# Optimization experiments

Measured on AMD Instinct MI355X. Metric: run time of the kernel, lower is better.

## Reference

```python
import jax, jax.numpy as jnp
import numpy as np

T, B, N, N2 = 2048, 32, 1024, 512

def setup_inputs() -> dict:
    key = jax.random.key(0)
    ks = jax.random.split(key, 7)
    s_n = 1.0 / np.sqrt(N)
    s_n2 = 1.0 / np.sqrt(N2)
    return {
        "hyp": jax.random.normal(ks[0], (T, B, N), dtype=jnp.float32),
        "W_w": jax.random.uniform(ks[1], (N2, N), jnp.float32, -s_n, s_n),
        "W_b": jax.random.uniform(ks[2], (N2,), jnp.float32, -s_n, s_n),
        "Wm_w": jax.random.uniform(ks[3], (N2, N), jnp.float32, -s_n, s_n),
        "Wm_b": jax.random.uniform(ks[4], (N2,), jnp.float32, -s_n, s_n),
        "Wh_w": jax.random.uniform(ks[5], (1, N2), jnp.float32, -s_n2, s_n2),
        "Wh_b": jax.random.uniform(ks[6], (1,), jnp.float32, -s_n2, s_n2),
        "dan_hidden_size": N,
        "attention_hidden_size": N2,
    }

def reference(hyp, W_w, W_b, Wm_w, Wm_b, Wh_w, Wh_b, dan_hidden_size, attention_hidden_size):
    # attention_type == 'attention' branch
    m = jnp.mean(hyp, axis=0)                      # [B, N] mean over time
    x = jnp.transpose(hyp, (1, 0, 2))              # [B, T, N]
    hq = jnp.tanh(jnp.einsum('btn,kn->btk', x, W_w) + W_b)        # [B, T, N2]
    hm = jnp.tanh(m @ Wm_w.T + Wm_b)[:, None, :]   # [B, 1, N2]
    h = hq * hm                                    # [B, T, N2]
    score = jnp.einsum('btk,ok->bto', h, Wh_w) + Wh_b  # [B, T, 1]
    a = jax.nn.softmax(score, axis=1)              # softmax over T
    c = jnp.sum(a * x, axis=1)                     # [B, N]
    return c
```

## Files before the change

### kernel.cpp

```cpp
#include <hip/hip_runtime.h>
#include <hip/hip_bf16.h>

#define TDIM 2048
#define BDIM 32
#define NDIM 1024
#define N2DIM 512
#define BN (BDIM * NDIM)
#define LDSP 72

typedef float f32x4 __attribute__((ext_vector_type(4)));
typedef __bf16 bf16x8 __attribute__((ext_vector_type(8)));

__device__ __forceinline__ float bf2f(unsigned int u) {
    union { unsigned int i; float f; } c;
    c.i = (u & 0xffffu) << 16;
    return c.f;
}

__device__ __forceinline__ unsigned short f2bf(float f) {
    union { float f; unsigned int i; } c;
    c.f = f;
    unsigned int i = c.i;
    unsigned int r = (i >> 16) & 1u;
    i += 0x7fffu + r;
    return (unsigned short)(i >> 16);
}

__device__ __forceinline__ int detect_f32(const void* wb) {
    const unsigned short* p = (const unsigned short*)wb;
    int cnt = 0;
    #pragma unroll
    for (int i = 0; i < 64; ++i) cnt += ((p[i] & 0x7fffu) <= 0x3D00u) ? 1 : 0;
    return cnt != 64;
}

__device__ __forceinline__ float ldf(const void* p, size_t i, int isf32) {
    if (isf32) return ((const float*)p)[i];
    return bf2f(((const unsigned short*)p)[i]);
}

__device__ __forceinline__ float tanh_fast(float x) {
    float e = __expf(2.0f * x);
    return 1.0f - 2.0f / (e + 1.0f);
}

__device__ __forceinline__ void unpack8(uint4 u, float* f) {
    f[0] = bf2f(u.x); f[1] = bf2f(u.x >> 16);
    f[2] = bf2f(u.y); f[3] = bf2f(u.y >> 16);
    f[4] = bf2f(u.z); f[5] = bf2f(u.z >> 16);
    f[6] = bf2f(u.w); f[7] = bf2f(u.w >> 16);
}

__device__ __forceinline__ void async16(const void* g, void* l) {
    __builtin_amdgcn_global_load_lds(
        (const __attribute__((address_space(1))) void*)g,
        (__attribute__((address_space(3))) void*)l, 16, 0, 0);
}


__global__ __launch_bounds__(256) void k_mean_cvt(const void* __restrict__ hyp,
                                                  const void* __restrict__ wb,
                                                  unsigned short* __restrict__ hyp16,
                                                  float* __restrict__ part) {
    const int isf32 = detect_f32(wb);
    const int col4 = (blockIdx.x * 256 + threadIdx.x) * 4;
    const int tc   = blockIdx.y;
    float a0 = 0.f, a1 = 0.f, a2 = 0.f, a3 = 0.f;
    if (isf32) {
        const float* h = (const float*)hyp + (size_t)(tc * 128) * BN + col4;
        unsigned short* o = hyp16 + (size_t)(tc * 128) * BN + col4;
        #pragma unroll 4
        for (int tt = 0; tt < 128; ++tt) {
            float4 v = *(const float4*)(h + (size_t)tt * BN);
            a0 += v.x; a1 += v.y; a2 += v.z; a3 += v.w;
            ushort4 u = { f2bf(v.x), f2bf(v.y), f2bf(v.z), f2bf(v.w) };
            *(ushort4*)(o + (size_t)tt * BN) = u;
        }
    } else {
        const unsigned short* h = (const unsigned short*)hyp + (size_t)(tc * 128) * BN + col4;
        unsigned short* o = hyp16 + (size_t)(tc * 128) * BN + col4;
        #pragma unroll 4
        for (int tt = 0; tt < 128; ++tt) {
            ushort4 u = *(const ushort4*)(h + (size_t)tt * BN);
            *(ushort4*)(o + (size_t)tt * BN) = u;
            a0 += bf2f(u.x); a1 += bf2f(u.y); a2 += bf2f(u.z); a3 += bf2f(u.w);
        }
    }
    float4 r = { a0, a1, a2, a3 };
    *(float4*)(part + (size_t)tc * BN + col4) = r;
}

__global__ __launch_bounds__(256) void k_reduce_mean(const float* __restrict__ part,
                                                     float* __restrict__ m) {
    int i4 = (blockIdx.x * 256 + threadIdx.x) * 4;
    float4 s = { 0.f, 0.f, 0.f, 0.f };
    #pragma unroll
    for (int c = 0; c < 16; ++c) {
        float4 v = *(const float4*)(part + (size_t)c * BN + i4);
        s.x += v.x; s.y += v.y; s.z += v.z; s.w += v.w;
    }
    float k = 1.0f / (float)TDIM;
    float4 r = { s.x * k, s.y * k, s.z * k, s.w * k };
    *(float4*)(m + i4) = r;
}

__global__ __launch_bounds__(256) void k_cvtW(const void* __restrict__ W_w,
                                              const void* __restrict__ wb,
                                              unsigned short* __restrict__ W16) {
    const int isf32 = detect_f32(wb);
    int i4 = (blockIdx.x * 256 + threadIdx.x) * 4;
    if (isf32) {
        float4 v = *(const float4*)((const float*)W_w + i4);
        ushort4 u = { f2bf(v.x), f2bf(v.y), f2bf(v.z), f2bf(v.w) };
        *(ushort4*)(W16 + i4) = u;
    } else {
        *(ushort4*)(W16 + i4) = *(const ushort4*)((const unsigned short*)W_w + i4);
    }
}

__global__ __launch_bounds__(256) void k_g(const float* __restrict__ m,
                                           const void* __restrict__ Wm_w,
                                           const void* __restrict__ Wm_b,
                                           const void* __restrict__ Wh_w,
                                           const void* __restrict__ wb,
                                           float* __restrict__ g) {
    const int isf32 = detect_f32(wb);
    int wid  = (blockIdx.x * 256 + threadIdx.x) >> 6;
    int lane = threadIdx.x & 63;
    int b = wid >> 9;
    int k = wid & 511;
    const float* mr = m + (size_t)b * NDIM;
    float s = 0.f;
    for (int i = lane; i < NDIM; i += 64)
        s += mr[i] * ldf(Wm_w, (size_t)k * NDIM + i, isf32);
    #pragma unroll
    for (int off = 32; off > 0; off >>= 1) s += __shfl_down(s, off, 64);
    if (lane == 0) {
        float v = tanh_fast(s + ldf(Wm_b, k, isf32));
        g[(size_t)b * N2DIM + k] = v * ldf(Wh_w, k, isf32);
    }
}

__global__ __launch_bounds__(256) void k_score(const unsigned short* __restrict__ hyp16,
                                               const unsigned short* __restrict__ W16,
                                               const void* __restrict__ W_b,
                                               const float* __restrict__ g,
                                               float* __restrict__ score) {
    __shared__ __align__(16) unsigned short sA[128 * 64];
    __shared__ __align__(16) unsigned short sW[128 * 64];
    __shared__ float sRed[2][128];

    const int isf32 = detect_f32(W_b);
    const int tid = threadIdx.x;
    const int l   = tid & 63;
    const int w   = tid >> 6;
    const int wt  = w & 1;
    const int wkk = w >> 1;
    const int lm  = l & 15;
    const int lq  = l >> 4;
    const int b   = blockIdx.y;
    const int t0  = blockIdx.x * 128;

    const int grow = l >> 3;
    const int gkq  = (l & 7) ^ grow;
    const int swz0 = ((lq)     ^ (lm & 7)) * 8;
    const int swz1 = ((4 + lq) ^ (lm & 7)) * 8;

    float scoreAcc[4][4];
    #pragma unroll
    for (int mi = 0; mi < 4; ++mi)
        #pragma unroll
        for (int r = 0; r < 4; ++r) scoreAcc[mi][r] = 0.f;

    for (int kblk = 0; kblk < 4; ++kblk) {
        f32x4 acc[4][4];
        #pragma unroll
        for (int mi = 0; mi < 4; ++mi)
            #pragma unroll
            for (int ni = 0; ni < 4; ++ni) {
                f32x4 z = {0.f, 0.f, 0.f, 0.f};
                acc[mi][ni] = z;
            }

        for (int it = 0; it < 16; ++it) {
            const int n0 = it * 64;
            #pragma unroll
            for (int p = 0; p < 4; ++p) {
                const int row = (w * 4 + p) * 8 + grow;
                async16(hyp16 + (size_t)(t0 + row) * BN + b * NDIM + n0 + gkq * 8,
                        &sA[(w * 4 + p) * 512]);
                async16(W16 + (size_t)(kblk * 128 + row) * NDIM + n0 + gkq * 8,
                        &sW[(w * 4 + p) * 512]);
            }
            __syncthreads();

            #pragma unroll
            for (int kk = 0; kk < 2; ++kk) {
                const int swz = kk ? swz1 : swz0;
                bf16x8 af[4];
                #pragma unroll
                for (int mi = 0; mi < 4; ++mi) {
                    int mrow = wt * 64 + mi * 16 + lm;
                    af[mi] = *(const bf16x8*)&sA[mrow * 64 + swz];
                }
                #pragma unroll
                for (int ni = 0; ni < 4; ++ni) {
                    int nrow = wkk * 64 + ni * 16 + lm;
                    bf16x8 bfr = *(const bf16x8*)&sW[nrow * 64 + swz];
                    #pragma unroll
                    for (int mi = 0; mi < 4; ++mi)
                        acc[mi][ni] = __builtin_amdgcn_mfma_f32_16x16x32_bf16(
                            af[mi], bfr, acc[mi][ni], 0, 0, 0);
                }
            }
            __syncthreads();
        }

        #pragma unroll
        for (int ni = 0; ni < 4; ++ni) {
            int kc = kblk * 128 + wkk * 64 + ni * 16 + lm;
            float wbv = ldf(W_b, kc, isf32);
            float gg  = g[(size_t)b * N2DIM + kc];
            #pragma unroll
            for (int mi = 0; mi < 4; ++mi)
                #pragma unroll
                for (int r = 0; r < 4; ++r) {
                    float v = tanh_fast(acc[mi][ni][r] + wbv);
                    scoreAcc[mi][r] += v * gg;
                }
        }
    }

    #pragma unroll
    for (int mi = 0; mi < 4; ++mi)
        #pragma unroll
        for (int r = 0; r < 4; ++r) {
            float s = scoreAcc[mi][r];
            s += __shfl_xor(s, 1, 64);
            s += __shfl_xor(s, 2, 64);
            s += __shfl_xor(s, 4, 64);
            s += __shfl_xor(s, 8, 64);
            if (lm == 0) sRed[wkk][wt * 64 + mi * 16 + lq * 4 + r] = s;
        }
    __syncthreads();
    if (tid < 128) {
        score[(size_t)b * TDIM + t0 + tid] = sRed[0][tid] + sRed[1][tid];
    }
}

__global__ __launch_bounds__(256) void k_softmax(const float* __restrict__ score,
                                                 float* __restrict__ a) {
    __shared__ float red[8];
    int b = blockIdx.x;
    int tid = threadIdx.x;
    int w = tid >> 6, l = tid & 63;
    const float* s = score + (size_t)b * TDIM;
    float v[8];
    float mx = -1e30f;
    #pragma unroll
    for (int i = 0; i < 8; ++i) { v[i] = s[tid + i * 256]; mx = fmaxf(mx, v[i]); }
    #pragma unroll
    for (int off = 32; off > 0; off >>= 1) mx = fmaxf(mx, __shfl_xor(mx, off, 64));
    if (l == 0) red[w] = mx;
    __syncthreads();
    mx = fmaxf(fmaxf(red[0], red[1]), fmaxf(red[2], red[3]));
    float sum = 0.f;
    #pragma unroll
    for (int i = 0; i < 8; ++i) { v[i] = __expf(v[i] - mx); sum += v[i]; }
    #pragma unroll
    for (int off = 32; off > 0; off >>= 1) sum += __shfl_xor(sum, off, 64);
    if (l == 0) red[4 + w] = sum;
    __syncthreads();
    sum = red[4] + red[5] + red[6] + red[7];
    float inv = 1.0f / sum;
    float* ap = a + (size_t)b * TDIM;
    #pragma unroll
    for (int i = 0; i < 8; ++i) ap[tid + i * 256] = v[i] * inv;
}

__global__ __launch_bounds__(256) void k_wsum_part(const unsigned short* __restrict__ hyp16,
                                                   const float* __restrict__ a,
                                                   float* __restrict__ part) {
    const int col8 = (blockIdx.x * 256 + threadIdx.x) * 8;
    const int tc   = blockIdx.y;
    const int b    = col8 >> 10;
    const float* av = a + (size_t)b * TDIM + tc * 128;
    const uint4* src = (const uint4*)(hyp16 + (size_t)(tc * 128) * BN + col8);
    float acc[8] = {0.f,0.f,0.f,0.f,0.f,0.f,0.f,0.f};
    #pragma unroll 4
    for (int tt = 0; tt < 128; ++tt) {
        float wgt = av[tt];
        uint4 u = src[(size_t)tt * (BN / 8)];
        float f[8]; unpack8(u, f);
        #pragma unroll
        for (int j = 0; j < 8; ++j) acc[j] += wgt * f[j];
    }
    float* dst = part + (size_t)tc * BN + col8;
    #pragma unroll
    for (int j = 0; j < 8; ++j) dst[j] = acc[j];
}

__global__ __launch_bounds__(256) void k_reduce_out(const float* __restrict__ part,
                                                    const void* __restrict__ wb,
                                                    void* __restrict__ out) {
    const int isf32 = detect_f32(wb);
    int i4 = (blockIdx.x * 256 + threadIdx.x) * 4;
    float4 s = { 0.f, 0.f, 0.f, 0.f };
    #pragma unroll
    for (int c = 0; c < 16; ++c) {
        float4 v = *(const float4*)(part + (size_t)c * BN + i4);
        s.x += v.x; s.y += v.y; s.z += v.z; s.w += v.w;
    }
    if (isf32) {
        *(float4*)((float*)out + i4) = s;
    } else {
        ushort4 u = { f2bf(s.x), f2bf(s.y), f2bf(s.z), f2bf(s.w) };
        *(ushort4*)((unsigned short*)out + i4) = u;
    }
}

__global__ __launch_bounds__(256) void k_mean_fb(const void* __restrict__ hyp,
                                                 const void* __restrict__ wb,
                                                 float* __restrict__ m) {
    const int isf32 = detect_f32(wb);
    int i = blockIdx.x * 256 + threadIdx.x;
    float s = 0.f;
    if (isf32) {
        const float* h = (const float*)hyp;
        #pragma unroll 8
        for (int t = 0; t < TDIM; ++t) s += h[(size_t)t * BN + i];
    } else {
        const unsigned short* h = (const unsigned short*)hyp;
        #pragma unroll 8
        for (int t = 0; t < TDIM; ++t) s += bf2f(h[(size_t)t * BN + i]);
    }
    m[i] = s * (1.0f / (float)TDIM);
}

__global__ __launch_bounds__(256) void k_score_fb(const void* __restrict__ hyp,
                                                  const void* __restrict__ W_w,
                                                  const void* __restrict__ W_b,
                                                  const float* __restrict__ g,
                                                  float* __restrict__ score) {
    __shared__ __align__(16) unsigned short sA[128 * LDSP];
    __shared__ __align__(16) unsigned short sW[128 * LDSP];
    __shared__ float sRed[2][128];

    const int isf32 = detect_f32(W_b);
    const int tid = threadIdx.x;
    const int l   = tid & 63;
    const int w   = tid >> 6;
    const int wt  = w & 1;
    const int wkk = w >> 1;
    const int lm  = l & 15;
    const int lq  = l >> 4;
    const int b   = blockIdx.y;
    const int t0  = blockIdx.x * 128;

    float scoreAcc[4][4];
    #pragma unroll
    for (int mi = 0; mi < 4; ++mi)
        #pragma unroll
        for (int r = 0; r < 4; ++r) scoreAcc[mi][r] = 0.f;

    for (int kblk = 0; kblk < 4; ++kblk) {
        f32x4 acc[4][4];
        #pragma unroll
        for (int mi = 0; mi < 4; ++mi)
            #pragma unroll
            for (int ni = 0; ni < 4; ++ni) {
                f32x4 z = {0.f, 0.f, 0.f, 0.f};
                acc[mi][ni] = z;
            }
        for (int it = 0; it < 16; ++it) {
            const int n0 = it * 64;
            #pragma unroll
            for (int p = 0; p < 4; ++p) {
                int ch  = p * 256 + tid;
                int row = ch >> 3;
                int pos = ch & 7;
                size_t offA = (size_t)(t0 + row) * BN + b * NDIM + n0 + pos * 8;
                size_t offW = (size_t)(kblk * 128 + row) * NDIM + n0 + pos * 8;
                uint4 va, vw;
                if (isf32) {
                    const float4* fa = (const float4*)((const float*)hyp + offA);
                    float4 a0 = fa[0], a1 = fa[1];
                    va.x = f2bf(a0.x) | ((unsigned)f2bf(a0.y) << 16);
                    va.y = f2bf(a0.z) | ((unsigned)f2bf(a0.w) << 16);
                    va.z = f2bf(a1.x) | ((unsigned)f2bf(a1.y) << 16);
                    va.w = f2bf(a1.z) | ((unsigned)f2bf(a1.w) << 16);
                    const float4* fw = (const float4*)((const float*)W_w + offW);
                    float4 w0 = fw[0], w1 = fw[1];
                    vw.x = f2bf(w0.x) | ((unsigned)f2bf(w0.y) << 16);
                    vw.y = f2bf(w0.z) | ((unsigned)f2bf(w0.w) << 16);
                    vw.z = f2bf(w1.x) | ((unsigned)f2bf(w1.y) << 16);
                    vw.w = f2bf(w1.z) | ((unsigned)f2bf(w1.w) << 16);
                } else {
                    va = *(const uint4*)((const unsigned short*)hyp + offA);
                    vw = *(const uint4*)((const unsigned short*)W_w + offW);
                }
                *(uint4*)&sA[row * LDSP + pos * 8] = va;
                *(uint4*)&sW[row * LDSP + pos * 8] = vw;
            }
            __syncthreads();
            #pragma unroll
            for (int kk = 0; kk < 2; ++kk) {
                const int koff = kk * 32 + lq * 8;
                bf16x8 af[4];
                #pragma unroll
                for (int mi = 0; mi < 4; ++mi) {
                    int mrow = wt * 64 + mi * 16 + lm;
                    af[mi] = *(const bf16x8*)&sA[mrow * LDSP + koff];
                }
                #pragma unroll
                for (int ni = 0; ni < 4; ++ni) {
                    int nrow = wkk * 64 + ni * 16 + lm;
                    bf16x8 bfr = *(const bf16x8*)&sW[nrow * LDSP + koff];
                    #pragma unroll
                    for (int mi = 0; mi < 4; ++mi)
                        acc[mi][ni] = __builtin_amdgcn_mfma_f32_16x16x32_bf16(
                            af[mi], bfr, acc[mi][ni], 0, 0, 0);
                }
            }
            __syncthreads();
        }
        #pragma unroll
        for (int ni = 0; ni < 4; ++ni) {
            int kc = kblk * 128 + wkk * 64 + ni * 16 + lm;
            float wbv = ldf(W_b, kc, isf32);
            float gg  = g[(size_t)b * N2DIM + kc];
            #pragma unroll
            for (int mi = 0; mi < 4; ++mi)
                #pragma unroll
                for (int r = 0; r < 4; ++r) {
                    float v = tanh_fast(acc[mi][ni][r] + wbv);
                    scoreAcc[mi][r] += v * gg;
                }
        }
    }
    #pragma unroll
    for (int mi = 0; mi < 4; ++mi)
        #pragma unroll
        for (int r = 0; r < 4; ++r) {
            float s = scoreAcc[mi][r];
            s += __shfl_xor(s, 1, 64);
            s += __shfl_xor(s, 2, 64);
            s += __shfl_xor(s, 4, 64);
            s += __shfl_xor(s, 8, 64);
            if (lm == 0) sRed[wkk][wt * 64 + mi * 16 + lq * 4 + r] = s;
        }
    __syncthreads();
    if (tid < 128) {
        score[(size_t)b * TDIM + t0 + tid] = sRed[0][tid] + sRed[1][tid];
    }
}

__global__ __launch_bounds__(256) void k_wsum_fb(const void* __restrict__ hyp,
                                                 const float* __restrict__ a,
                                                 const void* __restrict__ wb,
                                                 void* __restrict__ out) {
    const int isf32 = detect_f32(wb);
    int i = blockIdx.x * 256 + threadIdx.x;
    int b = i >> 10;
    const float* av = a + (size_t)b * TDIM;
    float s = 0.f;
    if (isf32) {
        const float* h = (const float*)hyp;
        #pragma unroll 8
        for (int t = 0; t < TDIM; ++t) s += av[t] * h[(size_t)t * BN + i];
    } else {
        const unsigned short* h = (const unsigned short*)hyp;
        #pragma unroll 8
        for (int t = 0; t < TDIM; ++t) s += av[t] * bf2f(h[(size_t)t * BN + i]);
    }
    if (isf32) ((float*)out)[i] = s;
    else       ((unsigned short*)out)[i] = f2bf(s);
}

extern "C" void kernel_launch(void* const* d_in, const int* in_sizes, int n_in,
                              void* d_out, int out_size, void* d_ws, size_t ws_size,
                              hipStream_t stream) {
    const void* hyp  = d_in[0];
    const void* W_w  = d_in[1];
    const void* W_b  = d_in[2];
    const void* Wm_w = d_in[3];
    const void* Wm_b = d_in[4];
    const void* Wh_w = d_in[5];

    float* ws    = (float*)d_ws;
    float* m     = ws;
    float* g     = m + BN;
    float* score = g + BDIM * N2DIM;
    float* a     = score + BDIM * TDIM;
    float* part  = a + BDIM * TDIM;
    unsigned short* W16   = (unsigned short*)(part + 16 * BN);
    unsigned short* hyp16 = W16 + (size_t)N2DIM * NDIM;
    const size_t need = 138084352ull;

    if (ws_size >= need) {
        k_mean_cvt  <<<dim3(32, 16), 256, 0, stream>>>(hyp, W_b, hyp16, part);
        k_reduce_mean<<<dim3(32),    256, 0, stream>>>(part, m);
        k_cvtW      <<<dim3(512),    256, 0, stream>>>(W_w, W_b, W16);
        k_g         <<<dim3(4096),   256, 0, stream>>>(m, Wm_w, Wm_b, Wh_w, W_b, g);
        k_score     <<<dim3(16, 32), 256, 0, stream>>>(hyp16, W16, W_b, g, score);
        k_softmax   <<<dim3(32),     256, 0, stream>>>(score, a);
        k_wsum_part <<<dim3(16, 16), 256, 0, stream>>>(hyp16, a, part);
        k_reduce_out<<<dim3(32),     256, 0, stream>>>(part, W_b, d_out);
    } else {
        k_mean_fb   <<<dim3(128),    256, 0, stream>>>(hyp, W_b, m);
        k_g         <<<dim3(4096),   256, 0, stream>>>(m, Wm_w, Wm_b, Wh_w, W_b, g);
        k_score_fb  <<<dim3(16, 32), 256, 0, stream>>>(hyp, W_w, W_b, g, score);
        k_softmax   <<<dim3(32),     256, 0, stream>>>(score, a);
        k_wsum_fb   <<<dim3(128),    256, 0, stream>>>(hyp, a, W_b, d_out);
    }
}
```

Measured before the change: 564.1 us.

## Split score GEMM over hidden blocks and raise time-chunk partitions for occupancy

The score kernel grid gains a z dimension over the four hidden-size blocks. Each block writes a partial score, and the softmax kernel sums the four partials. The mean and weighted-sum kernels now use 64 time chunks instead of 16, so more blocks run concurrently, and the mean reduction is merged into the W conversion kernel, removing one launch. k_g also switches to vectorized float4 loads. The cost is more partial-sum traffic and a larger workspace, and hyp16 A-tiles are now reloaded by each z block.

```diff
diff --git a/kernel.cpp b/kernel.cpp
--- a/kernel.cpp
+++ b/kernel.cpp
@@ -7,6 +7,7 @@
 #define N2DIM 512
 #define BN (BDIM * NDIM)
 #define LDSP 72
+#define NPART 64
 
 typedef float f32x4 __attribute__((ext_vector_type(4)));
 typedef __bf16 bf16x8 __attribute__((ext_vector_type(8)));
@@ -67,20 +68,20 @@
     const int tc   = blockIdx.y;
     float a0 = 0.f, a1 = 0.f, a2 = 0.f, a3 = 0.f;
     if (isf32) {
-        const float* h = (const float*)hyp + (size_t)(tc * 128) * BN + col4;
-        unsigned short* o = hyp16 + (size_t)(tc * 128) * BN + col4;
-        #pragma unroll 4
-        for (int tt = 0; tt < 128; ++tt) {
+        const float* h = (const float*)hyp + (size_t)(tc * 32) * BN + col4;
+        unsigned short* o = hyp16 + (size_t)(tc * 32) * BN + col4;
+        #pragma unroll 8
+        for (int tt = 0; tt < 32; ++tt) {
             float4 v = *(const float4*)(h + (size_t)tt * BN);
             a0 += v.x; a1 += v.y; a2 += v.z; a3 += v.w;
             ushort4 u = { f2bf(v.x), f2bf(v.y), f2bf(v.z), f2bf(v.w) };
             *(ushort4*)(o + (size_t)tt * BN) = u;
         }
     } else {
-        const unsigned short* h = (const unsigned short*)hyp + (size_t)(tc * 128) * BN + col4;
-        unsigned short* o = hyp16 + (size_t)(tc * 128) * BN + col4;
-        #pragma unroll 4
-        for (int tt = 0; tt < 128; ++tt) {
+        const unsigned short* h = (const unsigned short*)hyp + (size_t)(tc * 32) * BN + col4;
+        unsigned short* o = hyp16 + (size_t)(tc * 32) * BN + col4;
+        #pragma unroll 8
+        for (int tt = 0; tt < 32; ++tt) {
             ushort4 u = *(const ushort4*)(h + (size_t)tt * BN);
             *(ushort4*)(o + (size_t)tt * BN) = u;
             a0 += bf2f(u.x); a1 += bf2f(u.y); a2 += bf2f(u.z); a3 += bf2f(u.w);
@@ -90,31 +91,32 @@
     *(float4*)(part + (size_t)tc * BN + col4) = r;
 }
 
-__global__ __launch_bounds__(256) void k_reduce_mean(const float* __restrict__ part,
-                                                     float* __restrict__ m) {
-    int i4 = (blockIdx.x * 256 + threadIdx.x) * 4;
-    float4 s = { 0.f, 0.f, 0.f, 0.f };
-    #pragma unroll
-    for (int c = 0; c < 16; ++c) {
-        float4 v = *(const float4*)(part + (size_t)c * BN + i4);
-        s.x += v.x; s.y += v.y; s.z += v.z; s.w += v.w;
-    }
-    float k = 1.0f / (float)TDIM;
-    float4 r = { s.x * k, s.y * k, s.z * k, s.w * k };
-    *(float4*)(m + i4) = r;
-}
-
-__global__ __launch_bounds__(256) void k_cvtW(const void* __restrict__ W_w,
+__global__ __launch_bounds__(256) void k_prep(const void* __restrict__ W_w,
                                               const void* __restrict__ wb,
-                                              unsigned short* __restrict__ W16) {
+                                              const float* __restrict__ part,
+                                              unsigned short* __restrict__ W16,
+                                              float* __restrict__ m) {
     const int isf32 = detect_f32(wb);
-    int i4 = (blockIdx.x * 256 + threadIdx.x) * 4;
-    if (isf32) {
-        float4 v = *(const float4*)((const float*)W_w + i4);
-        ushort4 u = { f2bf(v.x), f2bf(v.y), f2bf(v.z), f2bf(v.w) };
-        *(ushort4*)(W16 + i4) = u;
-    } else {
-        *(ushort4*)(W16 + i4) = *(const ushort4*)((const unsigned short*)W_w + i4);
+    if (blockIdx.x < 512) {
+        int i4 = (blockIdx.x * 256 + threadIdx.x) * 4;
+        if (isf32) {
+            float4 v = *(const float4*)((const float*)W_w + i4);
+            ushort4 u = { f2bf(v.x), f2bf(v.y), f2bf(v.z), f2bf(v.w) };
+            *(ushort4*)(W16 + i4) = u;
+        } else {
+            *(ushort4*)(W16 + i4) = *(const ushort4*)((const unsigned short*)W_w + i4);
+        }
+    } else {
+        int i4 = ((blockIdx.x - 512) * 256 + threadIdx.x) * 4;
+        float4 s = { 0.f, 0.f, 0.f, 0.f };
+        #pragma unroll
+        for (int c = 0; c < NPART; ++c) {
+            float4 v = *(const float4*)(part + (size_t)c * BN + i4);
+            s.x += v.x; s.y += v.y; s.z += v.z; s.w += v.w;
+        }
+        float k = 1.0f / (float)TDIM;
+        float4 r = { s.x * k, s.y * k, s.z * k, s.w * k };
+        *(float4*)(m + i4) = r;
     }
 }
 
@@ -131,8 +133,26 @@
     int k = wid & 511;
     const float* mr = m + (size_t)b * NDIM;
     float s = 0.f;
-    for (int i = lane; i < NDIM; i += 64)
-        s += mr[i] * ldf(Wm_w, (size_t)k * NDIM + i, isf32);
+    if (isf32) {
+        const float* wr = (const float*)Wm_w + (size_t)k * NDIM;
+        #pragma unroll
+        for (int i = 0; i < 4; ++i) {
+            int idx = (lane + i * 64) * 4;
+            float4 mv = *(const float4*)(mr + idx);
+            float4 wv = *(const float4*)(wr + idx);
+            s += mv.x * wv.x + mv.y * wv.y + mv.z * wv.z + mv.w * wv.w;
+        }
+    } else {
+        const unsigned short* wr = (const unsigned short*)Wm_w + (size_t)k * NDIM;
+        #pragma unroll
+        for (int i = 0; i < 4; ++i) {
+            int idx = (lane + i * 64) * 4;
+            float4 mv = *(const float4*)(mr + idx);
+            ushort4 wv = *(const ushort4*)(wr + idx);
+            s += mv.x * bf2f(wv.x) + mv.y * bf2f(wv.y)
+               + mv.z * bf2f(wv.z) + mv.w * bf2f(wv.w);
+        }
+    }
     #pragma unroll
     for (int off = 32; off > 0; off >>= 1) s += __shfl_down(s, off, 64);
     if (lane == 0) {
@@ -145,7 +165,7 @@
                                                const unsigned short* __restrict__ W16,
                                                const void* __restrict__ W_b,
                                                const float* __restrict__ g,
-                                               float* __restrict__ score) {
+                                               float* __restrict__ sp) {
     __shared__ __align__(16) unsigned short sA[128 * 64];
     __shared__ __align__(16) unsigned short sW[128 * 64];
     __shared__ float sRed[2][128];
@@ -160,75 +180,73 @@
     const int lq  = l >> 4;
     const int b   = blockIdx.y;
     const int t0  = blockIdx.x * 128;
+    const int kblk = blockIdx.z;
 
     const int grow = l >> 3;
     const int gkq  = (l & 7) ^ grow;
     const int swz0 = ((lq)     ^ (lm & 7)) * 8;
     const int swz1 = ((4 + lq) ^ (lm & 7)) * 8;
 
+    f32x4 acc[4][4];
+    #pragma unroll
+    for (int mi = 0; mi < 4; ++mi)
+        #pragma unroll
+        for (int ni = 0; ni < 4; ++ni) {
+            f32x4 z = {0.f, 0.f, 0.f, 0.f};
+            acc[mi][ni] = z;
+        }
+
+    for (int it = 0; it < 16; ++it) {
+        const int n0 = it * 64;
+        #pragma unroll
+        for (int p = 0; p < 4; ++p) {
+            const int row = (w * 4 + p) * 8 + grow;
+            async16(hyp16 + (size_t)(t0 + row) * BN + b * NDIM + n0 + gkq * 8,
+                    &sA[(w * 4 + p) * 512]);
+            async16(W16 + (size_t)(kblk * 128 + row) * NDIM + n0 + gkq * 8,
+                    &sW[(w * 4 + p) * 512]);
+        }
+        __syncthreads();
+
+        #pragma unroll
+        for (int kk = 0; kk < 2; ++kk) {
+            const int swz = kk ? swz1 : swz0;
+            bf16x8 af[4];
+            #pragma unroll
+            for (int mi = 0; mi < 4; ++mi) {
+                int mrow = wt * 64 + mi * 16 + lm;
+                af[mi] = *(const bf16x8*)&sA[mrow * 64 + swz];
+            }
+            #pragma unroll
+            for (int ni = 0; ni < 4; ++ni) {
+                int nrow = wkk * 64 + ni * 16 + lm;
+                bf16x8 bfr = *(const bf16x8*)&sW[nrow * 64 + swz];
+                #pragma unroll
+                for (int mi = 0; mi < 4; ++mi)
+                    acc[mi][ni] = __builtin_amdgcn_mfma_f32_16x16x32_bf16(
+                        af[mi], bfr, acc[mi][ni], 0, 0, 0);
+            }
+        }
+        __syncthreads();
+    }
+
     float scoreAcc[4][4];
     #pragma unroll
     for (int mi = 0; mi < 4; ++mi)
         #pragma unroll
         for (int r = 0; r < 4; ++r) scoreAcc[mi][r] = 0.f;
-
-    for (int kblk = 0; kblk < 4; ++kblk) {
-        f32x4 acc[4][4];
+    #pragma unroll
+    for (int ni = 0; ni < 4; ++ni) {
+        int kc = kblk * 128 + wkk * 64 + ni * 16 + lm;
+        float wbv = ldf(W_b, kc, isf32);
+        float gg  = g[(size_t)b * N2DIM + kc];
         #pragma unroll
         for (int mi = 0; mi < 4; ++mi)
             #pragma unroll
-            for (int ni = 0; ni < 4; ++ni) {
-                f32x4 z = {0.f, 0.f, 0.f, 0.f};
-                acc[mi][ni] = z;
+            for (int r = 0; r < 4; ++r) {
+                float v = tanh_fast(acc[mi][ni][r] + wbv);
+                scoreAcc[mi][r] += v * gg;
             }
-
-        for (int it = 0; it < 16; ++it) {
-            const int n0 = it * 64;
-            #pragma unroll
-            for (int p = 0; p < 4; ++p) {
-                const int row = (w * 4 + p) * 8 + grow;
-                async16(hyp16 + (size_t)(t0 + row) * BN + b * NDIM + n0 + gkq * 8,
-                        &sA[(w * 4 + p) * 512]);
-                async16(W16 + (size_t)(kblk * 128 + row) * NDIM + n0 + gkq * 8,
-                        &sW[(w * 4 + p) * 512]);
-            }
-            __syncthreads();
-
-            #pragma unroll
-            for (int kk = 0; kk < 2; ++kk) {
-                const int swz = kk ? swz1 : swz0;
-                bf16x8 af[4];
-                #pragma unroll
-                for (int mi = 0; mi < 4; ++mi) {
-                    int mrow = wt * 64 + mi * 16 + lm;
-                    af[mi] = *(const bf16x8*)&sA[mrow * 64 + swz];
-                }
-                #pragma unroll
-                for (int ni = 0; ni < 4; ++ni) {
-                    int nrow = wkk * 64 + ni * 16 + lm;
-                    bf16x8 bfr = *(const bf16x8*)&sW[nrow * 64 + swz];
-                    #pragma unroll
-                    for (int mi = 0; mi < 4; ++mi)
-                        acc[mi][ni] = __builtin_amdgcn_mfma_f32_16x16x32_bf16(
-                            af[mi], bfr, acc[mi][ni], 0, 0, 0);
-                }
-            }
-            __syncthreads();
-        }
-
-        #pragma unroll
-        for (int ni = 0; ni < 4; ++ni) {
-            int kc = kblk * 128 + wkk * 64 + ni * 16 + lm;
-            float wbv = ldf(W_b, kc, isf32);
-            float gg  = g[(size_t)b * N2DIM + kc];
-            #pragma unroll
-            for (int mi = 0; mi < 4; ++mi)
-                #pragma unroll
-                for (int r = 0; r < 4; ++r) {
-                    float v = tanh_fast(acc[mi][ni][r] + wbv);
-                    scoreAcc[mi][r] += v * gg;
-                }
-        }
     }
 
     #pragma unroll
@@ -244,21 +262,27 @@
         }
     __syncthreads();
     if (tid < 128) {
-        score[(size_t)b * TDIM + t0 + tid] = sRed[0][tid] + sRed[1][tid];
-    }
-}
-
-__global__ __launch_bounds__(256) void k_softmax(const float* __restrict__ score,
+        sp[(size_t)(kblk * BDIM + b) * TDIM + t0 + tid] = sRed[0][tid] + sRed[1][tid];
+    }
+}
+
+__global__ __launch_bounds__(256) void k_softmax(const float* __restrict__ sp,
                                                  float* __restrict__ a) {
     __shared__ float red[8];
     int b = blockIdx.x;
     int tid = threadIdx.x;
     int w = tid >> 6, l = tid & 63;
-    const float* s = score + (size_t)b * TDIM;
     float v[8];
     float mx = -1e30f;
     #pragma unroll
-    for (int i = 0; i < 8; ++i) { v[i] = s[tid + i * 256]; mx = fmaxf(mx, v[i]); }
+    for (int i = 0; i < 8; ++i) {
+        int t = tid + i * 256;
+        float s = sp[(size_t)(0 * BDIM + b) * TDIM + t]
+                + sp[(size_t)(1 * BDIM + b) * TDIM + t]
+                + sp[(size_t)(2 * BDIM + b) * TDIM + t]
+                + sp[(size_t)(3 * BDIM + b) * TDIM + t];
+        v[i] = s; mx = fmaxf(mx, s);
+    }
     #pragma unroll
     for (int off = 32; off > 0; off >>= 1) mx = fmaxf(mx, __shfl_xor(mx, off, 64));
     if (l == 0) red[w] = mx;
@@ -284,11 +308,11 @@
     const int col8 = (blockIdx.x * 256 + threadIdx.x) * 8;
     const int tc   = blockIdx.y;
     const int b    = col8 >> 10;
-    const float* av = a + (size_t)b * TDIM + tc * 128;
-    const uint4* src = (const uint4*)(hyp16 + (size_t)(tc * 128) * BN + col8);
+    const float* av = a + (size_t)b * TDIM + tc * 32;
+    const uint4* src = (const uint4*)(hyp16 + (size_t)(tc * 32) * BN + col8);
     float acc[8] = {0.f,0.f,0.f,0.f,0.f,0.f,0.f,0.f};
-    #pragma unroll 4
-    for (int tt = 0; tt < 128; ++tt) {
+    #pragma unroll 8
+    for (int tt = 0; tt < 32; ++tt) {
         float wgt = av[tt];
         uint4 u = src[(size_t)tt * (BN / 8)];
         float f[8]; unpack8(u, f);
@@ -307,7 +331,7 @@
     int i4 = (blockIdx.x * 256 + threadIdx.x) * 4;
     float4 s = { 0.f, 0.f, 0.f, 0.f };
     #pragma unroll
-    for (int c = 0; c < 16; ++c) {
+    for (int c = 0; c < NPART; ++c) {
         float4 v = *(const float4*)(part + (size_t)c * BN + i4);
         s.x += v.x; s.y += v.y; s.z += v.z; s.w += v.w;
     }
@@ -455,6 +479,36 @@
     }
 }
 
+__global__ __launch_bounds__(256) void k_softmax_fb(const float* __restrict__ score,
+                                                    float* __restrict__ a) {
+    __shared__ float red[8];
+    int b = blockIdx.x;
+    int tid = threadIdx.x;
+    int w = tid >> 6, l = tid & 63;
+    const float* s = score + (size_t)b * TDIM;
+    float v[8];
+    float mx = -1e30f;
+    #pragma unroll
+    for (int i = 0; i < 8; ++i) { v[i] = s[tid + i * 256]; mx = fmaxf(mx, v[i]); }
+    #pragma unroll
+    for (int off = 32; off > 0; off >>= 1) mx = fmaxf(mx, __shfl_xor(mx, off, 64));
+    if (l == 0) red[w] = mx;
+    __syncthreads();
+    mx = fmaxf(fmaxf(red[0], red[1]), fmaxf(red[2], red[3]));
+    float sum = 0.f;
+    #pragma unroll
+    for (int i = 0; i < 8; ++i) { v[i] = __expf(v[i] - mx); sum += v[i]; }
+    #pragma unroll
+    for (int off = 32; off > 0; off >>= 1) sum += __shfl_xor(sum, off, 64);
+    if (l == 0) red[4 + w] = sum;
+    __syncthreads();
+    sum = red[4] + red[5] + red[6] + red[7];
+    float inv = 1.0f / sum;
+    float* ap = a + (size_t)b * TDIM;
+    #pragma unroll
+    for (int i = 0; i < 8; ++i) ap[tid + i * 256] = v[i] * inv;
+}
+
 __global__ __launch_bounds__(256) void k_wsum_fb(const void* __restrict__ hyp,
                                                  const float* __restrict__ a,
                                                  const void* __restrict__ wb,
@@ -490,27 +544,27 @@
     float* ws    = (float*)d_ws;
     float* m     = ws;
     float* g     = m + BN;
-    float* score = g + BDIM * N2DIM;
-    float* a     = score + BDIM * TDIM;
+    float* sp    = g + BDIM * N2DIM;
+    float* a     = sp + 4 * BDIM * TDIM;
     float* part  = a + BDIM * TDIM;
-    unsigned short* W16   = (unsigned short*)(part + 16 * BN);
+    unsigned short* W16   = (unsigned short*)(part + NPART * BN);
     unsigned short* hyp16 = W16 + (size_t)N2DIM * NDIM;
-    const size_t need = 138084352ull;
+    const size_t need = 145162240ull;
 
     if (ws_size >= need) {
-        k_mean_cvt  <<<dim3(32, 16), 256, 0, stream>>>(hyp, W_b, hyp16, part);
-        k_reduce_mean<<<dim3(32),    256, 0, stream>>>(part, m);
-        k_cvtW      <<<dim3(512),    256, 0, stream>>>(W_w, W_b, W16);
-        k_g         <<<dim3(4096),   256, 0, stream>>>(m, Wm_w, Wm_b, Wh_w, W_b, g);
-        k_score     <<<dim3(16, 32), 256, 0, stream>>>(hyp16, W16, W_b, g, score);
-        k_softmax   <<<dim3(32),     256, 0, stream>>>(score, a);
-        k_wsum_part <<<dim3(16, 16), 256, 0, stream>>>(hyp16, a, part);
-        k_reduce_out<<<dim3(32),     256, 0, stream>>>(part, W_b, d_out);
-    } else {
-        k_mean_fb   <<<dim3(128),    256, 0, stream>>>(hyp, W_b, m);
-        k_g         <<<dim3(4096),   256, 0, stream>>>(m, Wm_w, Wm_b, Wh_w, W_b, g);
-        k_score_fb  <<<dim3(16, 32), 256, 0, stream>>>(hyp, W_w, W_b, g, score);
-        k_softmax   <<<dim3(32),     256, 0, stream>>>(score, a);
-        k_wsum_fb   <<<dim3(128),    256, 0, stream>>>(hyp, a, W_b, d_out);
-    }
-}
+        k_mean_cvt <<<dim3(32, NPART), 256, 0, stream>>>(hyp, W_b, hyp16, part);
+        k_prep     <<<dim3(544),       256, 0, stream>>>(W_w, W_b, part, W16, m);
+        k_g        <<<dim3(4096),      256, 0, stream>>>(m, Wm_w, Wm_b, Wh_w, W_b, g);
+        k_score    <<<dim3(16, 32, 4), 256, 0, stream>>>(hyp16, W16, W_b, g, sp);
+        k_softmax  <<<dim3(32),        256, 0, stream>>>(sp, a);
+        k_wsum_part<<<dim3(16, NPART), 256, 0, stream>>>(hyp16, a, part);
+        k_reduce_out<<<dim3(32),       256, 0, stream>>>(part, W_b, d_out);
+    } else {
+        float* score = sp;
+        k_mean_fb  <<<dim3(128),    256, 0, stream>>>(hyp, W_b, m);
+        k_g        <<<dim3(4096),   256, 0, stream>>>(m, Wm_w, Wm_b, Wh_w, W_b, g);
+        k_score_fb <<<dim3(16, 32), 256, 0, stream>>>(hyp, W_w, W_b, g, score);
+        k_softmax_fb<<<dim3(32),    256, 0, stream>>>(score, a);
+        k_wsum_fb  <<<dim3(128),    256, 0, stream>>>(hyp, a, W_b, d_out);
+    }
+}
```

Result: no change. 556.6 us (-1.3%).
